# Kernel optimization log

Measured on AMD Instinct MI355X. Metric: run time of the kernel, lower is better.

The kernel has to match this reference:

```python
import jax, jax.numpy as jnp
import numpy as np

B, NE, NI, D = 256, 1024, 1024, 256  # batch, E cells, I cells, patch dim (16x16)
K_GAIN, N_EXP = 0.04, 2.0            # power-law i/o: k * relu(I)**n
TAU_E, TAU_I, DT = 0.02, 0.01, 0.001
STEPS, LAST_N = 200, 50              # int(T/dt) with T=0.2; average last 50 states
S_EE0, S_EI0, S_IE0, S_II0 = 3.75, 1.86, 3.13, 1.11 - 0.02
EPS = 1e-12
JEE, JEI, JIE, JII = 0.044, 0.023, 0.042, 0.018
SIGMA = 32.0


def ring_kernel(n_post, n_pre, sigma=SIGMA):
    post = np.linspace(0.0, 180.0, n_post + 1)[:-1]
    pre = np.linspace(0.0, 180.0, n_pre + 1)[:-1]
    d = np.abs(post[:, None] - pre[None, :])
    d = np.minimum(d, 180.0 - d)
    return np.exp(-(d * d) / (2.0 * sigma * sigma)).astype(np.float32)


def setup_inputs() -> dict:
    key = jax.random.key(0)
    kx, kE, kI = jax.random.split(key, 3)
    x_batch = jax.random.uniform(kx, (B, D), dtype=jnp.float32)
    W_EE = JEE * ring_kernel(NE, NE)
    np.fill_diagonal(W_EE, 0.0)
    W_EI = JEI * ring_kernel(NE, NI)
    W_IE = JIE * ring_kernel(NI, NE)
    W_II = JII * ring_kernel(NI, NI)
    np.fill_diagonal(W_II, 0.0)
    Wff_E = 0.1 * jax.random.uniform(kE, (NE, D), dtype=jnp.float32)
    Wff_E = Wff_E / (jnp.linalg.norm(Wff_E, axis=1, keepdims=True) + 1e-8)
    Wff_I = 0.1 * jax.random.uniform(kI, (NI, D), dtype=jnp.float32)
    Wff_I = Wff_I / (jnp.linalg.norm(Wff_I, axis=1, keepdims=True) + 1e-8)
    return {
        'x_batch': x_batch,
        'W_EE': jnp.asarray(W_EE), 'W_EI': jnp.asarray(W_EI),
        'W_IE': jnp.asarray(W_IE), 'W_II': jnp.asarray(W_II),
        'Wff_E': Wff_E, 'Wff_I': Wff_I,
    }


def powerlaw_io(I):
    return K_GAIN * jnp.maximum(I, 0.0) ** N_EXP


def reference(x_batch, W_EE, W_EI, W_IE, W_II, Wff_E, Wff_I):
    # per-postsynaptic current scalers (computed under no_grad in torch)
    gE_E = jax.lax.stop_gradient(S_EE0 / (W_EE.sum(axis=1) + EPS))
    gI_E = jax.lax.stop_gradient(S_EI0 / (W_EI.sum(axis=1) + EPS))
    gE_I = jax.lax.stop_gradient(S_IE0 / (W_IE.sum(axis=1) + EPS))
    gI_I = jax.lax.stop_gradient(S_II0 / (W_II.sum(axis=1) + EPS))
    # in-place clamp + rescale of weights (as in forward_dynamics)
    W_EE = jnp.minimum(W_EE, 0.15) * gE_E[:, None]
    W_EI = jnp.maximum(W_EI, 0.0005) * gI_E[:, None]
    W_IE = W_IE * gE_I[:, None]
    W_II = W_II * gI_I[:, None]

    Iff_E = x_batch @ Wff_E.T  # (B, nE)
    Iff_I = x_batch @ Wff_I.T  # (B, nI)

    def step(carry, t):
        rE, rI, accE, accI = carry
        IE = Iff_E + rE @ W_EE.T - rI @ W_EI.T
        II = Iff_I + rE @ W_IE.T - rI @ W_II.T
        rE = rE + (DT / TAU_E) * (-rE + powerlaw_io(IE))
        rI = rI + (DT / TAU_I) * (-rI + powerlaw_io(II))
        w = (t >= STEPS - LAST_N).astype(rE.dtype)
        return (rE, rI, accE + w * rE, accI + w * rI), None

    z = jnp.zeros((B, NE), dtype=x_batch.dtype)
    zi = jnp.zeros((B, NI), dtype=x_batch.dtype)
    (rE, rI, accE, accI), _ = jax.lax.scan(step, (z, zi, z, zi), jnp.arange(STEPS))
    rE_bar = accE / LAST_N
    rI_bar = accI / LAST_N
    return (rE_bar, rI_bar)
```

## Files before the change

kernel.cpp:

```cpp
#include <hip/hip_runtime.h>
#include <stdint.h>

typedef __attribute__((ext_vector_type(8))) _Float16 f16x8;
typedef __attribute__((ext_vector_type(8))) unsigned short u16x8;
typedef __attribute__((ext_vector_type(4))) float f32x4;

__device__ __forceinline__ float bf2f(unsigned short u) {
    union { uint32_t u; float f; } v; v.u = ((uint32_t)u) << 16; return v.f;
}
__device__ __forceinline__ unsigned short f2h(float f) {
    _Float16 h = (_Float16)f;
    return __builtin_bit_cast(unsigned short, h);
}
__device__ __forceinline__ f32x4 MFMAH(u16x8 a, u16x8 b, f32x4 c) {
    return __builtin_amdgcn_mfma_f32_16x16x32_f16(
        __builtin_bit_cast(f16x8, a), __builtin_bit_cast(f16x8, b), c, 0, 0, 0);
}

__device__ __forceinline__ int is_f32(const void* p) {
    const uint32_t* u = (const uint32_t*)p;
    int c = 0;
    #pragma unroll
    for (int i = 0; i < 64; i++) c += (u[i] >> 15) & 1;
    return c >= 4;
}
__device__ __forceinline__ float load_any(const void* base, size_t idx, int f32) {
    return f32 ? ((const float*)base)[idx] : bf2f(((const unsigned short*)base)[idx]);
}

__global__ void zero_kernel(float* __restrict__ p) {
    p[(size_t)blockIdx.x * 256 + threadIdx.x] = 0.0f;
}

__global__ void conv_kernel(const void* __restrict__ src, unsigned short* __restrict__ dst,
                            int clamp_wei) {
    int f32 = is_f32(src);
    size_t base = ((size_t)blockIdx.x * 256 + threadIdx.x) * 8;
    unsigned short v[8];
    if (f32) {
        const float* s = (const float*)src + base;
        #pragma unroll
        for (int e = 0; e < 8; e++) {
            float f = s[e];
            if (clamp_wei) f = fmaxf(f, 0.0005f);
            v[e] = f2h(f);
        }
    } else {
        const unsigned short* s = (const unsigned short*)src + base;
        #pragma unroll
        for (int e = 0; e < 8; e++) {
            float f = bf2f(s[e]);
            if (clamp_wei) f = fmaxf(f, 0.0005f);
            v[e] = f2h(f);
        }
    }
    *(u16x8*)(dst + base) = *(u16x8*)v;
}

__global__ void g_kernel(const void* __restrict__ WEE, const void* __restrict__ WEI,
                         const void* __restrict__ WIE, const void* __restrict__ WII,
                         float* __restrict__ gE, float* __restrict__ gI) {
    int i = blockIdx.x;
    int tid = threadIdx.x;
    const void* TE; const void* TI; float sEc, sIc; size_t row;
    if (i < 1024) { TE = WEE; TI = WEI; sEc = 3.75f; sIc = 1.86f; row = i; }
    else          { TE = WIE; TI = WII; sEc = 3.13f; sIc = (float)(1.11 - 0.02); row = i - 1024; }
    int fE = is_f32(TE), fI = is_f32(TI);
    float se = 0.f, si = 0.f;
    for (int j = tid; j < 1024; j += 256) {
        se += load_any(TE, row * 1024 + j, fE);
        si += load_any(TI, row * 1024 + j, fI);
    }
    for (int o = 32; o > 0; o >>= 1) { se += __shfl_down(se, o); si += __shfl_down(si, o); }
    __shared__ float lsE[4], lsI[4];
    int w = tid >> 6;
    if ((tid & 63) == 0) { lsE[w] = se; lsI[w] = si; }
    __syncthreads();
    if (tid == 0) {
        float te = lsE[0] + lsE[1] + lsE[2] + lsE[3];
        float ti = lsI[0] + lsI[1] + lsI[2] + lsI[3];
        gE[i] = sEc / (te + 1e-12f);
        gI[i] = sIc / (ti + 1e-12f);
    }
}

__global__ __launch_bounds__(256) void iff_kernel(const unsigned short* __restrict__ x,
                                                  const unsigned short* __restrict__ WffE,
                                                  const unsigned short* __restrict__ WffI,
                                                  float* __restrict__ Iff) {
    int n0 = blockIdx.x * 32;
    int m0 = blockIdx.y * 64;
    int tid = threadIdx.x, w = tid >> 6, lane = tid & 63;
    int l15 = lane & 15, quad = lane >> 4;
    int arow = m0 + 16 * w + l15;
    int nA = n0 + l15, nB = n0 + 16 + l15;
    const unsigned short* bA = (nA < 1024) ? (WffE + (size_t)nA * 256) : (WffI + (size_t)(nA - 1024) * 256);
    const unsigned short* bB = (nB < 1024) ? (WffE + (size_t)nB * 256) : (WffI + (size_t)(nB - 1024) * 256);
    f32x4 acc0 = {0.f, 0.f, 0.f, 0.f}, acc1 = {0.f, 0.f, 0.f, 0.f};
    #pragma unroll
    for (int ks = 0; ks < 8; ks++) {
        int k = ks * 32 + quad * 8;
        u16x8 a  = *(const u16x8*)(x + (size_t)arow * 256 + k);
        u16x8 b0 = *(const u16x8*)(bA + k);
        u16x8 b1 = *(const u16x8*)(bB + k);
        acc0 = MFMAH(a, b0, acc0);
        acc1 = MFMAH(a, b1, acc1);
    }
    #pragma unroll
    for (int v = 0; v < 4; v++) {
        int row = m0 + 16 * w + quad * 4 + v;
        Iff[(size_t)row * 2048 + n0 + l15]      = acc0[v];
        Iff[(size_t)row * 2048 + n0 + 16 + l15] = acc1[v];
    }
}

#define FLAG_STRIDE 32
__global__ __launch_bounds__(256, 1) void persist_kernel(
    const unsigned short* __restrict__ WEEc, const unsigned short* __restrict__ WEIc,
    const unsigned short* __restrict__ WIEc, const unsigned short* __restrict__ WIIc,
    unsigned short* __restrict__ h0, unsigned short* __restrict__ h1,
    const float* __restrict__ Iff, const float* __restrict__ gE, const float* __restrict__ gI,
    float* __restrict__ out, int* __restrict__ flags)
{
    __shared__ unsigned short Wl[32 * 2048];
    int bid = blockIdx.x;
    int nT = bid & 63;
    int mT = bid >> 6;
    int n0 = nT * 32;
    int m0 = mT * 64;
    int tid = threadIdx.x, w = tid >> 6, lane = tid & 63;
    int l15 = lane & 15, quad = lane >> 4;

    bool isEblk = (n0 < 1024);
    const unsigned short* W0 = isEblk ? WEEc : WIEc;
    const unsigned short* W1 = isEblk ? WEIc : WIIc;
    int nbase = n0 & 1023;

    {
        int k = tid * 8;
        const unsigned short* s0 = W0 + (size_t)nbase * 1024;
        const unsigned short* s1 = W1 + (size_t)nbase * 1024;
        #pragma unroll 4
        for (int row = 0; row < 32; row++) {
            const unsigned short* src = (k < 1024) ? (s0 + (size_t)row * 1024 + k)
                                                   : (s1 + (size_t)row * 1024 + (k - 1024));
            int gs = (tid + row) & 255;
            *(u16x8*)(Wl + row * 2048 + gs * 8) = *(const u16x8*)src;
        }
    }
    __syncthreads();

    int arow = m0 + 16 * w + l15;
    int colA = n0 + l15, colB = colA + 16;
    float invtau = isEblk ? 0.05f : 0.1f;
    float gEa = gE[colA], gIa = gI[colA], gEb = gE[colB], gIb = gI[colB];
    float iffA[4], iffB[4], rstA[4], rstB[4], sumA[4], sumB[4];
    int orow[4];
    #pragma unroll
    for (int v = 0; v < 4; v++) {
        orow[v] = m0 + 16 * w + quad * 4 + v;
        iffA[v] = Iff[(size_t)orow[v] * 2048 + colA];
        iffB[v] = Iff[(size_t)orow[v] * 2048 + colB];
        rstA[v] = 0.f; rstB[v] = 0.f; sumA[v] = 0.f; sumB[v] = 0.f;
    }

    const unsigned short* hi_in = h0;
    unsigned short* hi_out = h1;
    const unsigned short* WlA = Wl + l15 * 2048;
    const unsigned short* WlB = Wl + (16 + l15) * 2048;

    for (int t = 0; t < 200; t++) {
        const unsigned short* hp = hi_in + (size_t)arow * 2048;

        f32x4 eA0 = {0,0,0,0}, eA1 = {0,0,0,0}, eB0 = {0,0,0,0}, eB1 = {0,0,0,0};
        f32x4 iA0 = {0,0,0,0}, iA1 = {0,0,0,0}, iB0 = {0,0,0,0}, iB1 = {0,0,0,0};

        #pragma unroll 8
        for (int ks = 0; ks < 32; ks++) {
            int k = ks * 32 + quad * 8;
            int g = 4 * ks + quad;
            u16x8 a  = *(const u16x8*)(hp + k);
            u16x8 b0 = *(const u16x8*)(WlA + ((g + l15) & 255) * 8);
            u16x8 b1 = *(const u16x8*)(WlB + ((g + l15 + 16) & 255) * 8);
            if (ks & 1) { eA1 = MFMAH(a, b0, eA1); eB1 = MFMAH(a, b1, eB1); }
            else        { eA0 = MFMAH(a, b0, eA0); eB0 = MFMAH(a, b1, eB0); }
        }
        #pragma unroll 8
        for (int ks = 32; ks < 64; ks++) {
            int k = ks * 32 + quad * 8;
            int g = 4 * ks + quad;
            u16x8 a  = *(const u16x8*)(hp + k);
            u16x8 b0 = *(const u16x8*)(WlA + ((g + l15) & 255) * 8);
            u16x8 b1 = *(const u16x8*)(WlB + ((g + l15 + 16) & 255) * 8);
            if (ks & 1) { iA1 = MFMAH(a, b0, iA1); iB1 = MFMAH(a, b1, iB1); }
            else        { iA0 = MFMAH(a, b0, iA0); iB0 = MFMAH(a, b1, iB0); }
        }

        f32x4 aE0 = eA0 + eA1, aE1 = eB0 + eB1, aI0 = iA0 + iA1, aI1 = iB0 + iB1;

        float wacc = (t >= 150) ? 1.0f : 0.0f;
        #pragma unroll
        for (int v = 0; v < 4; v++) {
            size_t idx = (size_t)orow[v] * 2048;
            {
                float I = iffA[v] + gEa * aE0[v] - gIa * aI0[v];
                float rl = fmaxf(I, 0.f);
                float rnew = rstA[v] + invtau * (0.04f * rl * rl - rstA[v]);
                rstA[v] = rnew;
                __hip_atomic_store(hi_out + idx + colA, f2h(rnew),
                                   __ATOMIC_RELAXED, __HIP_MEMORY_SCOPE_AGENT);
                sumA[v] += wacc * rnew;
            }
            {
                float I = iffB[v] + gEb * aE1[v] - gIb * aI1[v];
                float rl = fmaxf(I, 0.f);
                float rnew = rstB[v] + invtau * (0.04f * rl * rl - rstB[v]);
                rstB[v] = rnew;
                __hip_atomic_store(hi_out + idx + colB, f2h(rnew),
                                   __ATOMIC_RELAXED, __HIP_MEMORY_SCOPE_AGENT);
                sumB[v] += wacc * rnew;
            }
        }

        __syncthreads();
        if (tid == 0) {
            __hip_atomic_store(&flags[bid * FLAG_STRIDE], t + 1,
                               __ATOMIC_RELAXED, __HIP_MEMORY_SCOPE_AGENT);
        }
        if (tid < 64) {
            const int fi = (mT * 64 + tid) * FLAG_STRIDE;
            while (__hip_atomic_load(&flags[fi], __ATOMIC_RELAXED,
                                     __HIP_MEMORY_SCOPE_AGENT) < t + 1) {
                __builtin_amdgcn_s_sleep(1);
            }
        }
        __syncthreads();
        if (tid == 0) {
            __builtin_amdgcn_fence(__ATOMIC_ACQUIRE, "agent");
        }
        __syncthreads();

        const unsigned short* th = hi_in; hi_in = hi_out; hi_out = (unsigned short*)th;
    }

    float* ob = out + (isEblk ? 0 : 262144);
    #pragma unroll
    for (int v = 0; v < 4; v++) {
        ob[(size_t)orow[v] * 1024 + nbase + l15]      = sumA[v] * (1.0f / 50.0f);
        ob[(size_t)orow[v] * 1024 + nbase + 16 + l15] = sumB[v] * (1.0f / 50.0f);
    }
}

extern "C" void kernel_launch(void* const* d_in, const int* in_sizes, int n_in,
                              void* d_out, int out_size, void* d_ws, size_t ws_size,
                              hipStream_t stream) {
    const void* x    = d_in[0];
    const void* WEE  = d_in[1];
    const void* WEI  = d_in[2];
    const void* WIE  = d_in[3];
    const void* WII  = d_in[4];
    const void* WffE = d_in[5];
    const void* WffI = d_in[6];

    char* ws = (char*)d_ws;
    const size_t MB = 1024 * 1024;
    const size_t KB = 1024;
    unsigned short* h0    = (unsigned short*)(ws + 0);
    int*            flags = (int*)(ws + 1 * MB);
    unsigned short* h1    = (unsigned short*)(ws + 2 * MB);
    float*          Iff   = (float*)(ws + 3 * MB);
    unsigned short* WEEc  = (unsigned short*)(ws + 5 * MB);
    unsigned short* WEIc  = (unsigned short*)(ws + 7 * MB);
    unsigned short* WIEc  = (unsigned short*)(ws + 9 * MB);
    unsigned short* WIIc  = (unsigned short*)(ws + 11 * MB);
    unsigned short* xc    = (unsigned short*)(ws + 13 * MB);
    unsigned short* WffEc = (unsigned short*)(ws + 13 * MB + 128 * KB);
    unsigned short* WffIc = (unsigned short*)(ws + 13 * MB + 640 * KB);
    float*          gE    = (float*)(ws + 13 * MB + 1152 * KB);
    float*          gI    = gE + 2048;

    zero_kernel<<<1056, 256, 0, stream>>>((float*)ws);

    conv_kernel<<<32,  256, 0, stream>>>(x,    xc,    0);
    conv_kernel<<<512, 256, 0, stream>>>(WEE,  WEEc,  0);
    conv_kernel<<<512, 256, 0, stream>>>(WEI,  WEIc,  1);
    conv_kernel<<<512, 256, 0, stream>>>(WIE,  WIEc,  0);
    conv_kernel<<<512, 256, 0, stream>>>(WII,  WIIc,  0);
    conv_kernel<<<128, 256, 0, stream>>>(WffE, WffEc, 0);
    conv_kernel<<<128, 256, 0, stream>>>(WffI, WffIc, 0);

    g_kernel<<<2048, 256, 0, stream>>>(WEE, WEI, WIE, WII, gE, gI);
    iff_kernel<<<dim3(64, 4), 256, 0, stream>>>(xc, WffEc, WffIc, Iff);

    float* outp = (float*)d_out;
    void* args[] = { &WEEc, &WEIc, &WIEc, &WIIc, &h0, &h1,
                     &Iff, &gE, &gI, &outp, &flags };
    hipLaunchCooperativeKernel((const void*)persist_kernel, dim3(256), dim3(256),
                               args, 0, stream);
}
```

Baseline: 2.575 ms.

## Pack barrier flags densely, drop acquire fence, use agent-scope atomic loads

```diff
diff --git a/kernel.cpp b/kernel.cpp
--- a/kernel.cpp
+++ b/kernel.cpp
@@ -3,6 +3,7 @@
 
 typedef __attribute__((ext_vector_type(8))) _Float16 f16x8;
 typedef __attribute__((ext_vector_type(8))) unsigned short u16x8;
+typedef __attribute__((ext_vector_type(2))) unsigned long long u64x2;
 typedef __attribute__((ext_vector_type(4))) float f32x4;
 
 __device__ __forceinline__ float bf2f(unsigned short u) {
@@ -15,6 +16,13 @@
 __device__ __forceinline__ f32x4 MFMAH(u16x8 a, u16x8 b, f32x4 c) {
     return __builtin_amdgcn_mfma_f32_16x16x32_f16(
         __builtin_bit_cast(f16x8, a), __builtin_bit_cast(f16x8, b), c, 0, 0, 0);
+}
+__device__ __forceinline__ u16x8 llc_load16(const unsigned short* p) {
+    const unsigned long long* q = (const unsigned long long*)p;
+    u64x2 c;
+    c.x = __hip_atomic_load(q,     __ATOMIC_RELAXED, __HIP_MEMORY_SCOPE_AGENT);
+    c.y = __hip_atomic_load(q + 1, __ATOMIC_RELAXED, __HIP_MEMORY_SCOPE_AGENT);
+    return __builtin_bit_cast(u16x8, c);
 }
 
 __device__ __forceinline__ int is_f32(const void* p) {
@@ -114,7 +122,6 @@
     }
 }
 
-#define FLAG_STRIDE 32
 __global__ __launch_bounds__(256, 1) void persist_kernel(
     const unsigned short* __restrict__ WEEc, const unsigned short* __restrict__ WEIc,
     const unsigned short* __restrict__ WIEc, const unsigned short* __restrict__ WIIc,
@@ -144,8 +151,7 @@
         for (int row = 0; row < 32; row++) {
             const unsigned short* src = (k < 1024) ? (s0 + (size_t)row * 1024 + k)
                                                    : (s1 + (size_t)row * 1024 + (k - 1024));
-            int gs = (tid + row) & 255;
-            *(u16x8*)(Wl + row * 2048 + gs * 8) = *(const u16x8*)src;
+            *(u16x8*)(Wl + row * 2048 + k) = *(const u16x8*)src;
         }
     }
     __syncthreads();
@@ -168,6 +174,8 @@
     unsigned short* hi_out = h1;
     const unsigned short* WlA = Wl + l15 * 2048;
     const unsigned short* WlB = Wl + (16 + l15) * 2048;
+    int* myflag = flags + mT * 64 + nT;
+    int* grpflags = flags + mT * 64;
 
     for (int t = 0; t < 200; t++) {
         const unsigned short* hp = hi_in + (size_t)arow * 2048;
@@ -178,20 +186,18 @@
         #pragma unroll 8
         for (int ks = 0; ks < 32; ks++) {
             int k = ks * 32 + quad * 8;
-            int g = 4 * ks + quad;
-            u16x8 a  = *(const u16x8*)(hp + k);
-            u16x8 b0 = *(const u16x8*)(WlA + ((g + l15) & 255) * 8);
-            u16x8 b1 = *(const u16x8*)(WlB + ((g + l15 + 16) & 255) * 8);
+            u16x8 a  = llc_load16(hp + k);
+            u16x8 b0 = *(const u16x8*)(WlA + k);
+            u16x8 b1 = *(const u16x8*)(WlB + k);
             if (ks & 1) { eA1 = MFMAH(a, b0, eA1); eB1 = MFMAH(a, b1, eB1); }
             else        { eA0 = MFMAH(a, b0, eA0); eB0 = MFMAH(a, b1, eB0); }
         }
         #pragma unroll 8
         for (int ks = 32; ks < 64; ks++) {
             int k = ks * 32 + quad * 8;
-            int g = 4 * ks + quad;
-            u16x8 a  = *(const u16x8*)(hp + k);
-            u16x8 b0 = *(const u16x8*)(WlA + ((g + l15) & 255) * 8);
-            u16x8 b1 = *(const u16x8*)(WlB + ((g + l15 + 16) & 255) * 8);
+            u16x8 a  = llc_load16(hp + k);
+            u16x8 b0 = *(const u16x8*)(WlA + k);
+            u16x8 b1 = *(const u16x8*)(WlB + k);
             if (ks & 1) { iA1 = MFMAH(a, b0, iA1); iB1 = MFMAH(a, b1, iB1); }
             else        { iA0 = MFMAH(a, b0, iA0); iB0 = MFMAH(a, b1, iB0); }
         }
@@ -224,19 +230,14 @@
 
         __syncthreads();
         if (tid == 0) {
-            __hip_atomic_store(&flags[bid * FLAG_STRIDE], t + 1,
+            __hip_atomic_store(myflag, t + 1,
                                __ATOMIC_RELAXED, __HIP_MEMORY_SCOPE_AGENT);
         }
         if (tid < 64) {
-            const int fi = (mT * 64 + tid) * FLAG_STRIDE;
-            while (__hip_atomic_load(&flags[fi], __ATOMIC_RELAXED,
+            while (__hip_atomic_load(grpflags + tid, __ATOMIC_RELAXED,
                                      __HIP_MEMORY_SCOPE_AGENT) < t + 1) {
                 __builtin_amdgcn_s_sleep(1);
             }
-        }
-        __syncthreads();
-        if (tid == 0) {
-            __builtin_amdgcn_fence(__ATOMIC_ACQUIRE, "agent");
         }
         __syncthreads();
 
@@ -279,7 +280,7 @@
     float*          gE    = (float*)(ws + 13 * MB + 1152 * KB);
     float*          gI    = gE + 2048;
 
-    zero_kernel<<<1056, 256, 0, stream>>>((float*)ws);
+    zero_kernel<<<1028, 256, 0, stream>>>((float*)ws);
 
     conv_kernel<<<32,  256, 0, stream>>>(x,    xc,    0);
     conv_kernel<<<512, 256, 0, stream>>>(WEE,  WEEc,  0);
```

Measured after the change: 3.970 ms. +54.2%, slower.

## Split persistent kernel into 512 blocks of 16 columns each

Applied to the files above, without the earlier changes.

```diff
diff --git a/kernel.cpp b/kernel.cpp
--- a/kernel.cpp
+++ b/kernel.cpp
@@ -114,19 +114,18 @@
     }
 }
 
-#define FLAG_STRIDE 32
-__global__ __launch_bounds__(256, 1) void persist_kernel(
+__global__ __launch_bounds__(256, 2) void persist_kernel(
     const unsigned short* __restrict__ WEEc, const unsigned short* __restrict__ WEIc,
     const unsigned short* __restrict__ WIEc, const unsigned short* __restrict__ WIIc,
     unsigned short* __restrict__ h0, unsigned short* __restrict__ h1,
     const float* __restrict__ Iff, const float* __restrict__ gE, const float* __restrict__ gI,
     float* __restrict__ out, int* __restrict__ flags)
 {
-    __shared__ unsigned short Wl[32 * 2048];
+    __shared__ unsigned short Wl[16 * 2048];
     int bid = blockIdx.x;
-    int nT = bid & 63;
-    int mT = bid >> 6;
-    int n0 = nT * 32;
+    int nT = bid & 127;
+    int mT = bid >> 7;
+    int n0 = nT * 16;
     int m0 = mT * 64;
     int tid = threadIdx.x, w = tid >> 6, lane = tid & 63;
     int l15 = lane & 15, quad = lane >> 4;
@@ -141,7 +140,7 @@
         const unsigned short* s0 = W0 + (size_t)nbase * 1024;
         const unsigned short* s1 = W1 + (size_t)nbase * 1024;
         #pragma unroll 4
-        for (int row = 0; row < 32; row++) {
+        for (int row = 0; row < 16; row++) {
             const unsigned short* src = (k < 1024) ? (s0 + (size_t)row * 1024 + k)
                                                    : (s1 + (size_t)row * 1024 + (k - 1024));
             int gs = (tid + row) & 255;
@@ -151,29 +150,29 @@
     __syncthreads();
 
     int arow = m0 + 16 * w + l15;
-    int colA = n0 + l15, colB = colA + 16;
+    int colA = n0 + l15;
     float invtau = isEblk ? 0.05f : 0.1f;
-    float gEa = gE[colA], gIa = gI[colA], gEb = gE[colB], gIb = gI[colB];
-    float iffA[4], iffB[4], rstA[4], rstB[4], sumA[4], sumB[4];
+    float gEa = gE[colA], gIa = gI[colA];
+    float iffA[4], rstA[4], sumA[4];
     int orow[4];
     #pragma unroll
     for (int v = 0; v < 4; v++) {
         orow[v] = m0 + 16 * w + quad * 4 + v;
         iffA[v] = Iff[(size_t)orow[v] * 2048 + colA];
-        iffB[v] = Iff[(size_t)orow[v] * 2048 + colB];
-        rstA[v] = 0.f; rstB[v] = 0.f; sumA[v] = 0.f; sumB[v] = 0.f;
+        rstA[v] = 0.f; sumA[v] = 0.f;
     }
 
     const unsigned short* hi_in = h0;
     unsigned short* hi_out = h1;
     const unsigned short* WlA = Wl + l15 * 2048;
-    const unsigned short* WlB = Wl + (16 + l15) * 2048;
+    int* myflag = flags + mT * 128 + nT;
+    int* grpflags = flags + mT * 128;
 
     for (int t = 0; t < 200; t++) {
         const unsigned short* hp = hi_in + (size_t)arow * 2048;
 
-        f32x4 eA0 = {0,0,0,0}, eA1 = {0,0,0,0}, eB0 = {0,0,0,0}, eB1 = {0,0,0,0};
-        f32x4 iA0 = {0,0,0,0}, iA1 = {0,0,0,0}, iB0 = {0,0,0,0}, iB1 = {0,0,0,0};
+        f32x4 eA0 = {0,0,0,0}, eA1 = {0,0,0,0};
+        f32x4 iA0 = {0,0,0,0}, iA1 = {0,0,0,0};
 
         #pragma unroll 8
         for (int ks = 0; ks < 32; ks++) {
@@ -181,9 +180,8 @@
             int g = 4 * ks + quad;
             u16x8 a  = *(const u16x8*)(hp + k);
             u16x8 b0 = *(const u16x8*)(WlA + ((g + l15) & 255) * 8);
-            u16x8 b1 = *(const u16x8*)(WlB + ((g + l15 + 16) & 255) * 8);
-            if (ks & 1) { eA1 = MFMAH(a, b0, eA1); eB1 = MFMAH(a, b1, eB1); }
-            else        { eA0 = MFMAH(a, b0, eA0); eB0 = MFMAH(a, b1, eB0); }
+            if (ks & 1) eA1 = MFMAH(a, b0, eA1);
+            else        eA0 = MFMAH(a, b0, eA0);
         }
         #pragma unroll 8
         for (int ks = 32; ks < 64; ks++) {
@@ -191,45 +189,32 @@
             int g = 4 * ks + quad;
             u16x8 a  = *(const u16x8*)(hp + k);
             u16x8 b0 = *(const u16x8*)(WlA + ((g + l15) & 255) * 8);
-            u16x8 b1 = *(const u16x8*)(WlB + ((g + l15 + 16) & 255) * 8);
-            if (ks & 1) { iA1 = MFMAH(a, b0, iA1); iB1 = MFMAH(a, b1, iB1); }
-            else        { iA0 = MFMAH(a, b0, iA0); iB0 = MFMAH(a, b1, iB0); }
-        }
-
-        f32x4 aE0 = eA0 + eA1, aE1 = eB0 + eB1, aI0 = iA0 + iA1, aI1 = iB0 + iB1;
+            if (ks & 1) iA1 = MFMAH(a, b0, iA1);
+            else        iA0 = MFMAH(a, b0, iA0);
+        }
+
+        f32x4 aE0 = eA0 + eA1, aI0 = iA0 + iA1;
 
         float wacc = (t >= 150) ? 1.0f : 0.0f;
         #pragma unroll
         for (int v = 0; v < 4; v++) {
             size_t idx = (size_t)orow[v] * 2048;
-            {
-                float I = iffA[v] + gEa * aE0[v] - gIa * aI0[v];
-                float rl = fmaxf(I, 0.f);
-                float rnew = rstA[v] + invtau * (0.04f * rl * rl - rstA[v]);
-                rstA[v] = rnew;
-                __hip_atomic_store(hi_out + idx + colA, f2h(rnew),
-                                   __ATOMIC_RELAXED, __HIP_MEMORY_SCOPE_AGENT);
-                sumA[v] += wacc * rnew;
-            }
-            {
-                float I = iffB[v] + gEb * aE1[v] - gIb * aI1[v];
-                float rl = fmaxf(I, 0.f);
-                float rnew = rstB[v] + invtau * (0.04f * rl * rl - rstB[v]);
-                rstB[v] = rnew;
-                __hip_atomic_store(hi_out + idx + colB, f2h(rnew),
-                                   __ATOMIC_RELAXED, __HIP_MEMORY_SCOPE_AGENT);
-                sumB[v] += wacc * rnew;
-            }
+            float I = iffA[v] + gEa * aE0[v] - gIa * aI0[v];
+            float rl = fmaxf(I, 0.f);
+            float rnew = rstA[v] + invtau * (0.04f * rl * rl - rstA[v]);
+            rstA[v] = rnew;
+            __hip_atomic_store(hi_out + idx + colA, f2h(rnew),
+                               __ATOMIC_RELAXED, __HIP_MEMORY_SCOPE_AGENT);
+            sumA[v] += wacc * rnew;
         }
 
         __syncthreads();
         if (tid == 0) {
-            __hip_atomic_store(&flags[bid * FLAG_STRIDE], t + 1,
+            __hip_atomic_store(myflag, t + 1,
                                __ATOMIC_RELAXED, __HIP_MEMORY_SCOPE_AGENT);
         }
-        if (tid < 64) {
-            const int fi = (mT * 64 + tid) * FLAG_STRIDE;
-            while (__hip_atomic_load(&flags[fi], __ATOMIC_RELAXED,
+        if (tid < 128) {
+            while (__hip_atomic_load(grpflags + tid, __ATOMIC_RELAXED,
                                      __HIP_MEMORY_SCOPE_AGENT) < t + 1) {
                 __builtin_amdgcn_s_sleep(1);
             }
@@ -246,8 +231,7 @@
     float* ob = out + (isEblk ? 0 : 262144);
     #pragma unroll
     for (int v = 0; v < 4; v++) {
-        ob[(size_t)orow[v] * 1024 + nbase + l15]      = sumA[v] * (1.0f / 50.0f);
-        ob[(size_t)orow[v] * 1024 + nbase + 16 + l15] = sumB[v] * (1.0f / 50.0f);
+        ob[(size_t)orow[v] * 1024 + nbase + l15] = sumA[v] * (1.0f / 50.0f);
     }
 }
 
@@ -279,7 +263,7 @@
     float*          gE    = (float*)(ws + 13 * MB + 1152 * KB);
     float*          gI    = gE + 2048;
 
-    zero_kernel<<<1056, 256, 0, stream>>>((float*)ws);
+    zero_kernel<<<1028, 256, 0, stream>>>((float*)ws);
 
     conv_kernel<<<32,  256, 0, stream>>>(x,    xc,    0);
     conv_kernel<<<512, 256, 0, stream>>>(WEE,  WEEc,  0);
@@ -295,6 +279,6 @@
     float* outp = (float*)d_out;
     void* args[] = { &WEEc, &WEIc, &WIEc, &WIIc, &h0, &h1,
                      &Iff, &gE, &gI, &outp, &flags };
-    hipLaunchCooperativeKernel((const void*)persist_kernel, dim3(256), dim3(256),
+    hipLaunchCooperativeKernel((const void*)persist_kernel, dim3(512), dim3(256),
                                args, 0, stream);
 }
```

Result: slower. 4.549 ms (+76.7%).

## Replace block barrier with per-wave flags and prefetch A rows into registers

Applied to the files above, without the earlier changes.

```diff
diff --git a/kernel.cpp b/kernel.cpp
--- a/kernel.cpp
+++ b/kernel.cpp
@@ -114,7 +114,6 @@
     }
 }
 
-#define FLAG_STRIDE 32
 __global__ __launch_bounds__(256, 1) void persist_kernel(
     const unsigned short* __restrict__ WEEc, const unsigned short* __restrict__ WEIc,
     const unsigned short* __restrict__ WIEc, const unsigned short* __restrict__ WIIc,
@@ -168,32 +167,36 @@
     unsigned short* hi_out = h1;
     const unsigned short* WlA = Wl + l15 * 2048;
     const unsigned short* WlB = Wl + (16 + l15) * 2048;
+    int* myflag = flags + mT * 256 + nT * 4 + w;
+    const int* gf = flags + mT * 256;
 
     for (int t = 0; t < 200; t++) {
         const unsigned short* hp = hi_in + (size_t)arow * 2048;
 
+        u16x8 areg[64];
+        #pragma unroll
+        for (int ks = 0; ks < 64; ks++) {
+            areg[ks] = *(const u16x8*)(hp + ks * 32 + quad * 8);
+        }
+
         f32x4 eA0 = {0,0,0,0}, eA1 = {0,0,0,0}, eB0 = {0,0,0,0}, eB1 = {0,0,0,0};
         f32x4 iA0 = {0,0,0,0}, iA1 = {0,0,0,0}, iB0 = {0,0,0,0}, iB1 = {0,0,0,0};
 
         #pragma unroll 8
         for (int ks = 0; ks < 32; ks++) {
-            int k = ks * 32 + quad * 8;
             int g = 4 * ks + quad;
-            u16x8 a  = *(const u16x8*)(hp + k);
             u16x8 b0 = *(const u16x8*)(WlA + ((g + l15) & 255) * 8);
             u16x8 b1 = *(const u16x8*)(WlB + ((g + l15 + 16) & 255) * 8);
-            if (ks & 1) { eA1 = MFMAH(a, b0, eA1); eB1 = MFMAH(a, b1, eB1); }
-            else        { eA0 = MFMAH(a, b0, eA0); eB0 = MFMAH(a, b1, eB0); }
+            if (ks & 1) { eA1 = MFMAH(areg[ks], b0, eA1); eB1 = MFMAH(areg[ks], b1, eB1); }
+            else        { eA0 = MFMAH(areg[ks], b0, eA0); eB0 = MFMAH(areg[ks], b1, eB0); }
         }
         #pragma unroll 8
         for (int ks = 32; ks < 64; ks++) {
-            int k = ks * 32 + quad * 8;
             int g = 4 * ks + quad;
-            u16x8 a  = *(const u16x8*)(hp + k);
             u16x8 b0 = *(const u16x8*)(WlA + ((g + l15) & 255) * 8);
             u16x8 b1 = *(const u16x8*)(WlB + ((g + l15 + 16) & 255) * 8);
-            if (ks & 1) { iA1 = MFMAH(a, b0, iA1); iB1 = MFMAH(a, b1, iB1); }
-            else        { iA0 = MFMAH(a, b0, iA0); iB0 = MFMAH(a, b1, iB0); }
+            if (ks & 1) { iA1 = MFMAH(areg[ks], b0, iA1); iB1 = MFMAH(areg[ks], b1, iB1); }
+            else        { iA0 = MFMAH(areg[ks], b0, iA0); iB0 = MFMAH(areg[ks], b1, iB0); }
         }
 
         f32x4 aE0 = eA0 + eA1, aE1 = eB0 + eB1, aI0 = iA0 + iA1, aI1 = iB0 + iB1;
@@ -222,23 +225,21 @@
             }
         }
 
-        __syncthreads();
-        if (tid == 0) {
-            __hip_atomic_store(&flags[bid * FLAG_STRIDE], t + 1,
+        __builtin_amdgcn_s_waitcnt(0);
+        if (lane == 0) {
+            __hip_atomic_store(myflag, t + 1,
                                __ATOMIC_RELAXED, __HIP_MEMORY_SCOPE_AGENT);
         }
-        if (tid < 64) {
-            const int fi = (mT * 64 + tid) * FLAG_STRIDE;
-            while (__hip_atomic_load(&flags[fi], __ATOMIC_RELAXED,
-                                     __HIP_MEMORY_SCOPE_AGENT) < t + 1) {
-                __builtin_amdgcn_s_sleep(1);
-            }
-        }
-        __syncthreads();
-        if (tid == 0) {
-            __builtin_amdgcn_fence(__ATOMIC_ACQUIRE, "agent");
-        }
-        __syncthreads();
+        for (;;) {
+            int f0 = __hip_atomic_load(gf + lane,       __ATOMIC_RELAXED, __HIP_MEMORY_SCOPE_AGENT);
+            int f1 = __hip_atomic_load(gf + lane + 64,  __ATOMIC_RELAXED, __HIP_MEMORY_SCOPE_AGENT);
+            int f2 = __hip_atomic_load(gf + lane + 128, __ATOMIC_RELAXED, __HIP_MEMORY_SCOPE_AGENT);
+            int f3 = __hip_atomic_load(gf + lane + 192, __ATOMIC_RELAXED, __HIP_MEMORY_SCOPE_AGENT);
+            int mn = min(min(f0, f1), min(f2, f3));
+            if (__all(mn >= t + 1)) break;
+            __builtin_amdgcn_s_sleep(1);
+        }
+        __builtin_amdgcn_fence(__ATOMIC_ACQUIRE, "agent");
 
         const unsigned short* th = hi_in; hi_in = hi_out; hi_out = (unsigned short*)th;
     }
@@ -279,7 +280,7 @@
     float*          gE    = (float*)(ws + 13 * MB + 1152 * KB);
     float*          gI    = gE + 2048;
 
-    zero_kernel<<<1056, 256, 0, stream>>>((float*)ws);
+    zero_kernel<<<1028, 256, 0, stream>>>((float*)ws);
 
     conv_kernel<<<32,  256, 0, stream>>>(x,    xc,    0);
     conv_kernel<<<512, 256, 0, stream>>>(WEE,  WEEc,  0);
```

Measured after the change: 8.604 ms. 234% more time.
